# Kernel optimization log

Hardware: AMD Instinct MI355X
Metric: run time of the kernel (lower is better)

## Reference

```python
import jax, jax.numpy as jnp
import numpy as np

EMBED_DIM = 768
NUM_HEADS = 12
HEAD_DIM = EMBED_DIM // NUM_HEADS
B, T = 2, 2048


def setup_inputs() -> dict:
    key = jax.random.key(0)
    ks = jax.random.split(key, 11)
    s = 1.0 / np.sqrt(EMBED_DIM)
    return {
        "query": jax.random.normal(ks[0], (B, T, EMBED_DIM), jnp.float32),
        "key_in": jax.random.normal(ks[1], (B, T, EMBED_DIM), jnp.float32),
        "value": jax.random.normal(ks[2], (B, T, EMBED_DIM), jnp.float32),
        "Wq": jax.random.uniform(ks[3], (EMBED_DIM, EMBED_DIM), jnp.float32, -s, s),
        "bq": jnp.zeros((EMBED_DIM,), jnp.float32),
        "Wk": jax.random.uniform(ks[4], (EMBED_DIM, EMBED_DIM), jnp.float32, -s, s),
        "bk": jnp.zeros((EMBED_DIM,), jnp.float32),
        "Wv": jax.random.uniform(ks[5], (EMBED_DIM, EMBED_DIM), jnp.float32, -s, s),
        "bv": jnp.zeros((EMBED_DIM,), jnp.float32),
        "Wo": jax.random.uniform(ks[6], (EMBED_DIM, EMBED_DIM), jnp.float32, -s, s),
        "bo": jnp.zeros((EMBED_DIM,), jnp.float32),
    }


def reference(query, key_in, value, Wq, bq, Wk, bk, Wv, bv, Wo, bo):
    b, t, _ = query.shape

    def split_heads(x):  # [B,T,E] -> [B,H,T,Dh]
        return x.reshape(b, t, NUM_HEADS, HEAD_DIM).transpose(0, 2, 1, 3)

    Q = split_heads(query @ Wq + bq)
    K = split_heads(key_in @ Wk + bk)
    V = split_heads(value @ Wv + bv)

    scores = jnp.einsum("bhqd,bhkd->bhqk", Q, K) / np.sqrt(HEAD_DIM).astype(np.float32)
    attn = jax.nn.softmax(scores, axis=-1)
    out = jnp.einsum("bhqk,bhkd->bhqd", attn, V)  # [B,H,T,Dh]
    out = out.transpose(0, 2, 1, 3).reshape(b, t, EMBED_DIM)
    return out @ Wo + bo
```

## Files before the change

### kernel.cpp

```cpp
#include <hip/hip_runtime.h>
#include <math.h>

typedef __attribute__((ext_vector_type(4))) float  floatx4;
typedef __attribute__((ext_vector_type(16))) float f32x16;
typedef __attribute__((ext_vector_type(8))) short  short8;
typedef __attribute__((ext_vector_type(4))) short  short4v;
typedef __attribute__((ext_vector_type(8))) __bf16 bf16x8;
typedef __attribute__((ext_vector_type(4))) unsigned int uint4v;

#define E_DIM 768
#define T_DIM 2048
#define N_B   2
#define N_H   12
#define H_D   64
#define M_TOT 4096

#define Q_SCALE 0.1803368801111204f

#if __has_builtin(__builtin_amdgcn_exp2f)
#define EXP2F(x) __builtin_amdgcn_exp2f(x)
#else
#define EXP2F(x) exp2f(x)
#endif
#if __has_builtin(__builtin_amdgcn_rcpf)
#define RCPF(x) __builtin_amdgcn_rcpf(x)
#else
#define RCPF(x) (1.0f / (x))
#endif

__device__ __forceinline__ unsigned short f32_to_bf16(float f) {
  unsigned int u = __float_as_uint(f);
  u += 0x7fffu + ((u >> 16) & 1u);
  return (unsigned short)(u >> 16);
}

__device__ __forceinline__ void lds_barrier() {
  asm volatile("s_waitcnt lgkmcnt(0)\n\ts_barrier" ::: "memory");
}

__device__ __forceinline__ void gload_lds16(const unsigned short* g, unsigned short* l) {
  __builtin_amdgcn_global_load_lds(
      (const __attribute__((address_space(1))) unsigned int*)(const void*)g,
      (__attribute__((address_space(3))) unsigned int*)(void*)l, 16, 0, 0);
}

__device__ __forceinline__ unsigned int cvtpk_bf16(float lo, float hi) {
  unsigned int r;
  asm("v_cvt_pk_bf16_f32 %0, %1, %2" : "=v"(r) : "v"(lo), "v"(hi));
  return r;
}

__device__ __forceinline__ void perml32_swap(unsigned int& a, unsigned int& b) {
  asm volatile("v_permlane32_swap_b32 %0, %1" : "+v"(a), "+v"(b));
}

__global__ __launch_bounds__(256) void convert_x(const float* __restrict__ q,
                                                 const float* __restrict__ k,
                                                 const float* __restrict__ v,
                                                 unsigned short* __restrict__ Xb) {
  const int z = blockIdx.y;
  const float* src = (z == 0) ? q : (z == 1) ? k : v;
  size_t idx = ((size_t)blockIdx.x * 256 + threadIdx.x) * 4;
  float4 val = *reinterpret_cast<const float4*>(&src[idx]);
  short4v o;
  o[0] = (short)f32_to_bf16(val.x);
  o[1] = (short)f32_to_bf16(val.y);
  o[2] = (short)f32_to_bf16(val.z);
  o[3] = (short)f32_to_bf16(val.w);
  *reinterpret_cast<short4v*>(&Xb[(size_t)z * M_TOT * E_DIM + idx]) = o;
}

__global__ __launch_bounds__(256) void transpose_w4(const float* __restrict__ W0,
                                                    const float* __restrict__ W1,
                                                    const float* __restrict__ W2,
                                                    const float* __restrict__ W3,
                                                    unsigned short* __restrict__ Wt) {
  __shared__ float tile[32][33];
  const int z = blockIdx.z;
  const float* W = (z == 0) ? W0 : (z == 1) ? W1 : (z == 2) ? W2 : W3;
  unsigned short* dst = Wt + (size_t)z * E_DIM * E_DIM;
  int k0 = blockIdx.x * 32, n0 = blockIdx.y * 32;
  int tx = threadIdx.x & 31, ty = threadIdx.x >> 5;
  for (int i = 0; i < 4; i++)
    tile[ty + i * 8][tx] = W[(size_t)(k0 + ty + i * 8) * E_DIM + n0 + tx];
  __syncthreads();
  for (int i = 0; i < 4; i++)
    dst[(size_t)(n0 + ty + i * 8) * E_DIM + k0 + tx] = f32_to_bf16(tile[tx][ty + i * 8]);
}

__global__ __launch_bounds__(256) void gemm_qkv(const unsigned short* __restrict__ Xb,
                                                const unsigned short* __restrict__ WtAll,
                                                const float* __restrict__ bq,
                                                const float* __restrict__ bk,
                                                const float* __restrict__ bv,
                                                unsigned short* __restrict__ outQKV) {
  __shared__ unsigned short As[128 * 32];
  __shared__ unsigned short Bs[128 * 32];

  const int z = blockIdx.z;
  const unsigned short* A = Xb + (size_t)z * M_TOT * E_DIM;
  const float* bias = (z == 0) ? bq : (z == 1) ? bk : bv;
  const unsigned short* W = WtAll + (size_t)z * E_DIM * E_DIM;
  unsigned short* out = outQKV + (size_t)z * M_TOT * E_DIM;
  const float scale = (z == 0) ? Q_SCALE : 1.0f;

  const int tid = threadIdx.x;
  const int lane = tid & 63, wv = tid >> 6;
  const int m15 = lane & 15, quad = lane >> 4;
  const int wm = (wv & 1) * 64, wn = (wv >> 1) * 64;
  const int m0 = blockIdx.x * 128, n0 = blockIdx.y * 128;

  floatx4 acc[4][4] = {};
  const int srow = lane >> 2, scol = (lane & 3) * 8;

  for (int k0 = 0; k0 < E_DIM; k0 += 32) {
    for (int cc = 0; cc < 2; cc++) {
      int c = wv * 2 + cc;
      gload_lds16(&A[(size_t)(m0 + c * 16 + srow) * E_DIM + k0 + scol], &As[c * 512]);
      gload_lds16(&W[(size_t)(n0 + c * 16 + srow) * E_DIM + k0 + scol], &Bs[c * 512]);
    }
    __syncthreads();
    bf16x8 af[4], bfr[4];
    for (int i = 0; i < 4; i++)
      af[i] = *reinterpret_cast<const bf16x8*>(&As[(wm + i * 16 + m15) * 32 + quad * 8]);
    for (int j = 0; j < 4; j++)
      bfr[j] = *reinterpret_cast<const bf16x8*>(&Bs[(wn + j * 16 + m15) * 32 + quad * 8]);
    for (int i = 0; i < 4; i++)
      for (int j = 0; j < 4; j++)
        acc[i][j] = __builtin_amdgcn_mfma_f32_16x16x32_bf16(af[i], bfr[j], acc[i][j], 0, 0, 0);
    __syncthreads();
  }

  for (int i = 0; i < 4; i++)
    for (int j = 0; j < 4; j++) {
      int gn = n0 + wn + j * 16 + m15;
      int h = gn >> 6, d = gn & 63;
      float bso = bias[gn];
      for (int r = 0; r < 4; r++) {
        int gm = m0 + wm + i * 16 + quad * 4 + r;
        int bb = gm >> 11, tt = gm & 2047;
        float v = (acc[i][j][r] + bso) * scale;
        out[(((size_t)bb * N_H + h) * T_DIM + tt) * H_D + d] = f32_to_bf16(v);
      }
    }
}

__global__ __launch_bounds__(256) void transpose_v(const unsigned short* __restrict__ Vg_all,
                                                   unsigned short* __restrict__ VT) {
  __shared__ unsigned short tile[64 * 72];
  const int t0 = blockIdx.x * 64, h = blockIdx.y, bb = blockIdx.z;
  const unsigned short* Vg = Vg_all + (((size_t)bb * N_H + h) * T_DIM) * H_D;
  unsigned short* VTh = VT + (((size_t)bb * N_H + h) * H_D) * T_DIM;
  const int tid = threadIdx.x;
  const int tloc = tid & 63, d0 = (tid >> 6) * 16;

  short8 r0 = *reinterpret_cast<const short8*>(&Vg[(size_t)(t0 + tloc) * H_D + d0]);
  short8 r1 = *reinterpret_cast<const short8*>(&Vg[(size_t)(t0 + tloc) * H_D + d0 + 8]);
#pragma unroll
  for (int j = 0; j < 8; j++) {
    tile[(d0 + j) * 72 + tloc] = (unsigned short)r0[j];
    tile[(d0 + 8 + j) * 72 + tloc] = (unsigned short)r1[j];
  }
  __syncthreads();
  const int d = tid >> 2, ts = (tid & 3) * 16;
  short8 w0 = *reinterpret_cast<const short8*>(&tile[d * 72 + ts]);
  short8 w1 = *reinterpret_cast<const short8*>(&tile[d * 72 + ts + 8]);
  *reinterpret_cast<short8*>(&VTh[(size_t)d * T_DIM + t0 + ts]) = w0;
  *reinterpret_cast<short8*>(&VTh[(size_t)d * T_DIM + t0 + ts + 8]) = w1;
}

__global__ __launch_bounds__(64, 1) void attn(const unsigned short* __restrict__ QKV,
                                              const unsigned short* __restrict__ VT,
                                              unsigned short* __restrict__ ctx) {
  __shared__ unsigned short Ks[2][64 * 64];
  __shared__ unsigned short Vs[2][64 * 64];

  const int qt = blockIdx.x, h = blockIdx.y, bb = blockIdx.z;
  const size_t headoff = (((size_t)bb * N_H + h) * T_DIM) * H_D;
  const unsigned short* Qg = QKV + headoff;
  const unsigned short* Kg = QKV + (size_t)M_TOT * E_DIM + headoff;
  const unsigned short* VTg = VT + (((size_t)bb * N_H + h) * H_D) * T_DIM;

  const int lane = threadIdx.x;
  const int l31 = lane & 31, hi = lane >> 5, l7 = lane & 7;
  const int q0 = qt * 64;

  const int srow = lane >> 3;
  const int sslot = (lane & 7) ^ srow;
  const unsigned short* gK = Kg + (size_t)srow * H_D + sslot * 8;
  const unsigned short* gV = VTg + (size_t)srow * T_DIM + sslot * 8;

  bf16x8 aqA[4], aqB[4];
#pragma unroll
  for (int c = 0; c < 4; c++) {
    aqA[c] = *reinterpret_cast<const bf16x8*>(&Qg[(size_t)(q0 + l31) * H_D + c * 16 + hi * 8]);
    aqB[c] = *reinterpret_cast<const bf16x8*>(&Qg[(size_t)(q0 + 32 + l31) * H_D + c * 16 + hi * 8]);
  }

#pragma unroll
  for (int i = 0; i < 8; i++) {
    gload_lds16(gK + (size_t)(i * 8) * H_D, &Ks[0][i * 512]);
    gload_lds16(gV + (size_t)(i * 8) * T_DIM, &Vs[0][i * 512]);
  }
#pragma unroll
  for (int i = 0; i < 8; i++) {
    gload_lds16(gK + (size_t)(64 + i * 8) * H_D, &Ks[1][i * 512]);
    gload_lds16(gV + (size_t)(i * 8) * T_DIM + 64, &Vs[1][i * 512]);
  }
  asm volatile("s_waitcnt vmcnt(16)" ::: "memory");

  f32x16 oA0 = {}, oA1 = {}, oB0 = {}, oB1 = {};
  float laccA = 0.f, laccB = 0.f;
  bf16x8 paA0[2], paA1[2], paB0[2], paB1[2];

  auto QK = [&](const unsigned short* kb, f32x16& a0, f32x16& a1, f32x16& b0, f32x16& b1) {
#pragma unroll
    for (int c = 0; c < 4; c++) {
      const int slot = ((c << 1) | hi) ^ l7;
      bf16x8 k0 = *reinterpret_cast<const bf16x8*>(&kb[l31 * 64 + slot * 8]);
      bf16x8 k1 = *reinterpret_cast<const bf16x8*>(&kb[(32 + l31) * 64 + slot * 8]);
      a0 = __builtin_amdgcn_mfma_f32_32x32x16_bf16(k0, aqA[c], a0, 0, 0, 0);
      a1 = __builtin_amdgcn_mfma_f32_32x32x16_bf16(k1, aqA[c], a1, 0, 0, 0);
      b0 = __builtin_amdgcn_mfma_f32_32x32x16_bf16(k0, aqB[c], b0, 0, 0, 0);
      b1 = __builtin_amdgcn_mfma_f32_32x32x16_bf16(k1, aqB[c], b1, 0, 0, 0);
    }
  };
  auto PV = [&](const unsigned short* vb) {
#pragma unroll
    for (int cc = 0; cc < 2; cc++) {
      const int sl0 = ((cc << 1) | hi) ^ l7;
      const int sl1 = (4 + (cc << 1) + hi) ^ l7;
      bf16x8 v00 = *reinterpret_cast<const bf16x8*>(&vb[l31 * 64 + sl0 * 8]);
      bf16x8 v01 = *reinterpret_cast<const bf16x8*>(&vb[(32 + l31) * 64 + sl0 * 8]);
      bf16x8 v10 = *reinterpret_cast<const bf16x8*>(&vb[l31 * 64 + sl1 * 8]);
      bf16x8 v11 = *reinterpret_cast<const bf16x8*>(&vb[(32 + l31) * 64 + sl1 * 8]);
      oA0 = __builtin_amdgcn_mfma_f32_32x32x16_bf16(paA0[cc], v00, oA0, 0, 0, 0);
      oA1 = __builtin_amdgcn_mfma_f32_32x32x16_bf16(paA0[cc], v01, oA1, 0, 0, 0);
      oA0 = __builtin_amdgcn_mfma_f32_32x32x16_bf16(paA1[cc], v10, oA0, 0, 0, 0);
      oA1 = __builtin_amdgcn_mfma_f32_32x32x16_bf16(paA1[cc], v11, oA1, 0, 0, 0);
      oB0 = __builtin_amdgcn_mfma_f32_32x32x16_bf16(paB0[cc], v00, oB0, 0, 0, 0);
      oB1 = __builtin_amdgcn_mfma_f32_32x32x16_bf16(paB0[cc], v01, oB1, 0, 0, 0);
      oB0 = __builtin_amdgcn_mfma_f32_32x32x16_bf16(paB1[cc], v10, oB0, 0, 0, 0);
      oB1 = __builtin_amdgcn_mfma_f32_32x32x16_bf16(paB1[cc], v11, oB1, 0, 0, 0);
    }
  };
  auto PACK1 = [&](f32x16& s0, f32x16& s1, float& lacc, bf16x8* pl, bf16x8* ph) {
#pragma unroll
    for (int i = 0; i < 16; i++) { s0[i] = EXP2F(s0[i]); s1[i] = EXP2F(s1[i]); }
    float a0 = 0.f, a1 = 0.f, a2 = 0.f, a3 = 0.f;
#pragma unroll
    for (int i = 0; i < 16; i += 4) {
      a0 += s0[i]; a1 += s0[i + 1]; a2 += s0[i + 2]; a3 += s0[i + 3];
      a0 += s1[i]; a1 += s1[i + 1]; a2 += s1[i + 2]; a3 += s1[i + 3];
    }
    lacc += (a0 + a1) + (a2 + a3);
#pragma unroll
    for (int cc = 0; cc < 2; cc++) {
      {
        unsigned int x0 = cvtpk_bf16(s0[8 * cc + 0], s0[8 * cc + 1]);
        unsigned int x1 = cvtpk_bf16(s0[8 * cc + 2], s0[8 * cc + 3]);
        unsigned int y0 = cvtpk_bf16(s0[8 * cc + 4], s0[8 * cc + 5]);
        unsigned int y1 = cvtpk_bf16(s0[8 * cc + 6], s0[8 * cc + 7]);
        perml32_swap(x0, y0);
        perml32_swap(x1, y1);
        uint4v u; u[0] = x0; u[1] = x1; u[2] = y0; u[3] = y1;
        pl[cc] = __builtin_bit_cast(bf16x8, u);
      }
      {
        unsigned int x0 = cvtpk_bf16(s1[8 * cc + 0], s1[8 * cc + 1]);
        unsigned int x1 = cvtpk_bf16(s1[8 * cc + 2], s1[8 * cc + 3]);
        unsigned int y0 = cvtpk_bf16(s1[8 * cc + 4], s1[8 * cc + 5]);
        unsigned int y1 = cvtpk_bf16(s1[8 * cc + 6], s1[8 * cc + 7]);
        perml32_swap(x0, y0);
        perml32_swap(x1, y1);
        uint4v u; u[0] = x0; u[1] = x1; u[2] = y0; u[3] = y1;
        ph[cc] = __builtin_bit_cast(bf16x8, u);
      }
    }
  };

  {
    f32x16 sA0 = {}, sA1 = {}, sB0 = {}, sB1 = {};
    __builtin_amdgcn_s_setprio(1);
    QK(Ks[0], sA0, sA1, sB0, sB1);
    __builtin_amdgcn_s_setprio(0);
    asm volatile("s_waitcnt lgkmcnt(0)" ::: "memory");
#pragma unroll
    for (int i = 0; i < 8; i++)
      gload_lds16(gK + (size_t)(128 + i * 8) * H_D, &Ks[0][i * 512]);
    PACK1(sA0, sA1, laccA, paA0, paA1);
    PACK1(sB0, sB1, laccB, paB0, paB1);
    asm volatile("s_waitcnt vmcnt(8)" ::: "memory");
  }

  for (int kt = 1; kt <= 30; ++kt) {
    f32x16 sA0 = {}, sA1 = {}, sB0 = {}, sB1 = {};
    __builtin_amdgcn_s_setprio(1);
    QK(Ks[kt & 1], sA0, sA1, sB0, sB1);
    PV(Vs[(kt - 1) & 1]);
    __builtin_amdgcn_s_setprio(0);
    asm volatile("s_waitcnt lgkmcnt(0)" ::: "memory");
    if (kt < 30) {
      const int nk = kt + 2;
#pragma unroll
      for (int i = 0; i < 8; i++)
        gload_lds16(gK + (size_t)(nk * 64 + i * 8) * H_D, &Ks[kt & 1][i * 512]);
    }
    {
      const int nv = kt + 1;
#pragma unroll
      for (int i = 0; i < 8; i++)
        gload_lds16(gV + (size_t)(i * 8) * T_DIM + nv * 64, &Vs[nv & 1][i * 512]);
    }
    PACK1(sA0, sA1, laccA, paA0, paA1);
    PACK1(sB0, sB1, laccB, paB0, paB1);
    if (kt < 30) asm volatile("s_waitcnt vmcnt(16)" ::: "memory");
    else         asm volatile("s_waitcnt vmcnt(8)" ::: "memory");
  }

  {
    f32x16 sA0 = {}, sA1 = {}, sB0 = {}, sB1 = {};
    __builtin_amdgcn_s_setprio(1);
    QK(Ks[1], sA0, sA1, sB0, sB1);
    PV(Vs[0]);
    __builtin_amdgcn_s_setprio(0);
    PACK1(sA0, sA1, laccA, paA0, paA1);
    PACK1(sB0, sB1, laccB, paB0, paB1);
    asm volatile("s_waitcnt vmcnt(0)" ::: "memory");
    __builtin_amdgcn_s_setprio(1);
    PV(Vs[1]);
    __builtin_amdgcn_s_setprio(0);
  }

  float ltA = laccA + __shfl_xor(laccA, 32, 64);
  float rlA = RCPF(ltA);
  float ltB = laccB + __shfl_xor(laccB, 32, 64);
  float rlB = RCPF(ltB);
  const size_t obase = ((size_t)bb * T_DIM + q0) * E_DIM + (size_t)h * H_D;
#pragma unroll
  for (int r = 0; r < 16; r++) {
    const int qr = (r & 3) + 8 * (r >> 2) + 4 * hi;
    float ra = __shfl(rlA, qr, 64);
    ctx[obase + (size_t)qr * E_DIM + l31]      = f32_to_bf16(oA0[r] * ra);
    ctx[obase + (size_t)qr * E_DIM + 32 + l31] = f32_to_bf16(oA1[r] * ra);
    float rb = __shfl(rlB, qr, 64);
    ctx[obase + (size_t)(32 + qr) * E_DIM + l31]      = f32_to_bf16(oB0[r] * rb);
    ctx[obase + (size_t)(32 + qr) * E_DIM + 32 + l31] = f32_to_bf16(oB1[r] * rb);
  }
}

__global__ __launch_bounds__(256) void gemm_out(const unsigned short* __restrict__ Actx,
                                                const unsigned short* __restrict__ Wt,
                                                const float* __restrict__ bias,
                                                float* __restrict__ out) {
  __shared__ unsigned short As[64 * 32];
  __shared__ unsigned short Bs[128 * 32];

  const int tid = threadIdx.x;
  const int lane = tid & 63, wv = tid >> 6;
  const int m15 = lane & 15, quad = lane >> 4;
  const int wm = (wv & 1) * 32, wn = (wv >> 1) * 64;
  const int m0 = blockIdx.x * 64, n0 = blockIdx.y * 128;

  floatx4 acc[2][4] = {};
  const int srow = lane >> 2, scol = (lane & 3) * 8;

  for (int k0 = 0; k0 < E_DIM; k0 += 32) {
    gload_lds16(&Actx[(size_t)(m0 + wv * 16 + srow) * E_DIM + k0 + scol], &As[wv * 512]);
    for (int cc = 0; cc < 2; cc++) {
      int c = wv * 2 + cc;
      gload_lds16(&Wt[(size_t)(n0 + c * 16 + srow) * E_DIM + k0 + scol], &Bs[c * 512]);
    }
    __syncthreads();
    bf16x8 af[2], bfr[4];
    for (int i = 0; i < 2; i++)
      af[i] = *reinterpret_cast<const bf16x8*>(&As[(wm + i * 16 + m15) * 32 + quad * 8]);
    for (int j = 0; j < 4; j++)
      bfr[j] = *reinterpret_cast<const bf16x8*>(&Bs[(wn + j * 16 + m15) * 32 + quad * 8]);
    for (int i = 0; i < 2; i++)
      for (int j = 0; j < 4; j++)
        acc[i][j] = __builtin_amdgcn_mfma_f32_16x16x32_bf16(af[i], bfr[j], acc[i][j], 0, 0, 0);
    __syncthreads();
  }

  for (int i = 0; i < 2; i++)
    for (int j = 0; j < 4; j++) {
      int gn = n0 + wn + j * 16 + m15;
      float bso = bias[gn];
      for (int r = 0; r < 4; r++) {
        int gm = m0 + wm + i * 16 + quad * 4 + r;
        out[(size_t)gm * E_DIM + gn] = acc[i][j][r] + bso;
      }
    }
}

extern "C" void kernel_launch(void* const* d_in, const int* in_sizes, int n_in,
                              void* d_out, int out_size, void* d_ws, size_t ws_size,
                              hipStream_t stream) {
  const float* query  = (const float*)d_in[0];
  const float* key_in = (const float*)d_in[1];
  const float* value  = (const float*)d_in[2];
  const float* Wq = (const float*)d_in[3];
  const float* bq = (const float*)d_in[4];
  const float* Wk = (const float*)d_in[5];
  const float* bk = (const float*)d_in[6];
  const float* Wv = (const float*)d_in[7];
  const float* bv = (const float*)d_in[8];
  const float* Wo = (const float*)d_in[9];
  const float* bo = (const float*)d_in[10];
  float* out = (float*)d_out;

  unsigned short* ws  = (unsigned short*)d_ws;
  unsigned short* Wt  = ws;
  unsigned short* Xb  = Wt + (size_t)4 * E_DIM * E_DIM;
  unsigned short* QKV = Xb + (size_t)3 * M_TOT * E_DIM;
  unsigned short* VT  = QKV + (size_t)3 * M_TOT * E_DIM;
  unsigned short* ctx = VT + (size_t)N_B * N_H * H_D * T_DIM;

  dim3 tb(256);
  convert_x<<<dim3(M_TOT * E_DIM / 1024, 3), tb, 0, stream>>>(query, key_in, value, Xb);
  transpose_w4<<<dim3(24, 24, 4), tb, 0, stream>>>(Wq, Wk, Wv, Wo, Wt);

  gemm_qkv<<<dim3(32, 6, 3), tb, 0, stream>>>(Xb, Wt, bq, bk, bv, QKV);
  transpose_v<<<dim3(32, 12, 2), tb, 0, stream>>>(QKV + (size_t)2 * M_TOT * E_DIM, VT);
  attn<<<dim3(32, 12, 2), dim3(64), 0, stream>>>(QKV, VT, ctx);
  gemm_out<<<dim3(64, 6), tb, 0, stream>>>(ctx, Wt + (size_t)3 * E_DIM * E_DIM, bo, out);
  (void)in_sizes; (void)n_in; (void)out_size; (void)ws_size;
}
```

Measured before the change: 198.1 us.

## Split attention KV range across two blocks with atomic accumulation and combine kernel

Each attention block now covers only half of the key/value tiles, so twice as many single-wave blocks are launched to fill more of the GPU. Partial unnormalized outputs and row sums are accumulated into fp32 buffers with atomicAdd. A new combine kernel then normalizes the result and converts it to bf16 for the output GEMM. The fp32 buffer is zeroed inside the V-transpose kernel and reuses the Xb workspace. The cost is extra atomic traffic, a zeroing pass and one more kernel launch. The approach relies on the softmax not using a per-block running max, so the two halves add linearly.

```diff
diff --git a/kernel.cpp b/kernel.cpp
--- a/kernel.cpp
+++ b/kernel.cpp
@@ -14,6 +14,8 @@
 #define N_H   12
 #define H_D   64
 #define M_TOT 4096
+
+#define KV_TILES_PER_BLOCK 16
 
 #define Q_SCALE 0.1803368801111204f
 
@@ -32,10 +34,6 @@
   unsigned int u = __float_as_uint(f);
   u += 0x7fffu + ((u >> 16) & 1u);
   return (unsigned short)(u >> 16);
-}
-
-__device__ __forceinline__ void lds_barrier() {
-  asm volatile("s_waitcnt lgkmcnt(0)\n\ts_barrier" ::: "memory");
 }
 
 __device__ __forceinline__ void gload_lds16(const unsigned short* g, unsigned short* l) {
@@ -146,7 +144,8 @@
 }
 
 __global__ __launch_bounds__(256) void transpose_v(const unsigned short* __restrict__ Vg_all,
-                                                   unsigned short* __restrict__ VT) {
+                                                   unsigned short* __restrict__ VT,
+                                                   float* __restrict__ Oz) {
   __shared__ unsigned short tile[64 * 72];
   const int t0 = blockIdx.x * 64, h = blockIdx.y, bb = blockIdx.z;
   const unsigned short* Vg = Vg_all + (((size_t)bb * N_H + h) * T_DIM) * H_D;
@@ -154,6 +153,14 @@
   const int tid = threadIdx.x;
   const int tloc = tid & 63, d0 = (tid >> 6) * 16;
 
+  {
+    const unsigned int gid = ((blockIdx.z * (unsigned)N_H + blockIdx.y) * 32 + blockIdx.x) * 256 + tid;
+    float4* Z = reinterpret_cast<float4*>(Oz);
+    const float4 z4 = {0.f, 0.f, 0.f, 0.f};
+    for (size_t i = gid; i < (size_t)((M_TOT * E_DIM + M_TOT * N_H) / 4); i += 196608)
+      Z[i] = z4;
+  }
+
   short8 r0 = *reinterpret_cast<const short8*>(&Vg[(size_t)(t0 + tloc) * H_D + d0]);
   short8 r1 = *reinterpret_cast<const short8*>(&Vg[(size_t)(t0 + tloc) * H_D + d0 + 8]);
 #pragma unroll
@@ -171,11 +178,14 @@
 
 __global__ __launch_bounds__(64, 1) void attn(const unsigned short* __restrict__ QKV,
                                               const unsigned short* __restrict__ VT,
-                                              unsigned short* __restrict__ ctx) {
+                                              float* __restrict__ O,
+                                              float* __restrict__ L) {
   __shared__ unsigned short Ks[2][64 * 64];
   __shared__ unsigned short Vs[2][64 * 64];
 
-  const int qt = blockIdx.x, h = blockIdx.y, bb = blockIdx.z;
+  const int qt = blockIdx.x, h = blockIdx.y;
+  const int bb = blockIdx.z >> 1, half = blockIdx.z & 1;
+  const int tb = half * KV_TILES_PER_BLOCK;
   const size_t headoff = (((size_t)bb * N_H + h) * T_DIM) * H_D;
   const unsigned short* Qg = QKV + headoff;
   const unsigned short* Kg = QKV + (size_t)M_TOT * E_DIM + headoff;
@@ -199,13 +209,13 @@
 
 #pragma unroll
   for (int i = 0; i < 8; i++) {
-    gload_lds16(gK + (size_t)(i * 8) * H_D, &Ks[0][i * 512]);
-    gload_lds16(gV + (size_t)(i * 8) * T_DIM, &Vs[0][i * 512]);
+    gload_lds16(gK + (size_t)((tb + 0) * 64 + i * 8) * H_D, &Ks[0][i * 512]);
+    gload_lds16(gV + (size_t)(i * 8) * T_DIM + (tb + 0) * 64, &Vs[0][i * 512]);
   }
 #pragma unroll
   for (int i = 0; i < 8; i++) {
-    gload_lds16(gK + (size_t)(64 + i * 8) * H_D, &Ks[1][i * 512]);
-    gload_lds16(gV + (size_t)(i * 8) * T_DIM + 64, &Vs[1][i * 512]);
+    gload_lds16(gK + (size_t)((tb + 1) * 64 + i * 8) * H_D, &Ks[1][i * 512]);
+    gload_lds16(gV + (size_t)(i * 8) * T_DIM + (tb + 1) * 64, &Vs[1][i * 512]);
   }
   asm volatile("s_waitcnt vmcnt(16)" ::: "memory");
 
@@ -287,66 +297,84 @@
     asm volatile("s_waitcnt lgkmcnt(0)" ::: "memory");
 #pragma unroll
     for (int i = 0; i < 8; i++)
-      gload_lds16(gK + (size_t)(128 + i * 8) * H_D, &Ks[0][i * 512]);
+      gload_lds16(gK + (size_t)((tb + 2) * 64 + i * 8) * H_D, &Ks[0][i * 512]);
     PACK1(sA0, sA1, laccA, paA0, paA1);
     PACK1(sB0, sB1, laccB, paB0, paB1);
     asm volatile("s_waitcnt vmcnt(8)" ::: "memory");
   }
 
-  for (int kt = 1; kt <= 30; ++kt) {
+  for (int kt = 1; kt <= KV_TILES_PER_BLOCK - 2; ++kt) {
     f32x16 sA0 = {}, sA1 = {}, sB0 = {}, sB1 = {};
     __builtin_amdgcn_s_setprio(1);
     QK(Ks[kt & 1], sA0, sA1, sB0, sB1);
     PV(Vs[(kt - 1) & 1]);
     __builtin_amdgcn_s_setprio(0);
     asm volatile("s_waitcnt lgkmcnt(0)" ::: "memory");
-    if (kt < 30) {
+    if (kt < KV_TILES_PER_BLOCK - 2) {
       const int nk = kt + 2;
 #pragma unroll
       for (int i = 0; i < 8; i++)
-        gload_lds16(gK + (size_t)(nk * 64 + i * 8) * H_D, &Ks[kt & 1][i * 512]);
+        gload_lds16(gK + (size_t)((tb + nk) * 64 + i * 8) * H_D, &Ks[kt & 1][i * 512]);
     }
     {
       const int nv = kt + 1;
 #pragma unroll
       for (int i = 0; i < 8; i++)
-        gload_lds16(gV + (size_t)(i * 8) * T_DIM + nv * 64, &Vs[nv & 1][i * 512]);
+        gload_lds16(gV + (size_t)(i * 8) * T_DIM + (tb + nv) * 64, &Vs[nv & 1][i * 512]);
     }
     PACK1(sA0, sA1, laccA, paA0, paA1);
     PACK1(sB0, sB1, laccB, paB0, paB1);
-    if (kt < 30) asm volatile("s_waitcnt vmcnt(16)" ::: "memory");
-    else         asm volatile("s_waitcnt vmcnt(8)" ::: "memory");
+    if (kt < KV_TILES_PER_BLOCK - 2)
+      asm volatile("s_waitcnt vmcnt(16)" ::: "memory");
+    else
+      asm volatile("s_waitcnt vmcnt(8)" ::: "memory");
   }
 
   {
     f32x16 sA0 = {}, sA1 = {}, sB0 = {}, sB1 = {};
     __builtin_amdgcn_s_setprio(1);
-    QK(Ks[1], sA0, sA1, sB0, sB1);
-    PV(Vs[0]);
+    QK(Ks[(KV_TILES_PER_BLOCK - 1) & 1], sA0, sA1, sB0, sB1);
+    PV(Vs[(KV_TILES_PER_BLOCK - 2) & 1]);
     __builtin_amdgcn_s_setprio(0);
     PACK1(sA0, sA1, laccA, paA0, paA1);
     PACK1(sB0, sB1, laccB, paB0, paB1);
     asm volatile("s_waitcnt vmcnt(0)" ::: "memory");
     __builtin_amdgcn_s_setprio(1);
-    PV(Vs[1]);
+    PV(Vs[(KV_TILES_PER_BLOCK - 1) & 1]);
     __builtin_amdgcn_s_setprio(0);
   }
 
   float ltA = laccA + __shfl_xor(laccA, 32, 64);
-  float rlA = RCPF(ltA);
   float ltB = laccB + __shfl_xor(laccB, 32, 64);
-  float rlB = RCPF(ltB);
   const size_t obase = ((size_t)bb * T_DIM + q0) * E_DIM + (size_t)h * H_D;
 #pragma unroll
   for (int r = 0; r < 16; r++) {
     const int qr = (r & 3) + 8 * (r >> 2) + 4 * hi;
-    float ra = __shfl(rlA, qr, 64);
-    ctx[obase + (size_t)qr * E_DIM + l31]      = f32_to_bf16(oA0[r] * ra);
-    ctx[obase + (size_t)qr * E_DIM + 32 + l31] = f32_to_bf16(oA1[r] * ra);
-    float rb = __shfl(rlB, qr, 64);
-    ctx[obase + (size_t)(32 + qr) * E_DIM + l31]      = f32_to_bf16(oB0[r] * rb);
-    ctx[obase + (size_t)(32 + qr) * E_DIM + 32 + l31] = f32_to_bf16(oB1[r] * rb);
-  }
+    atomicAdd(&O[obase + (size_t)qr * E_DIM + l31], oA0[r]);
+    atomicAdd(&O[obase + (size_t)qr * E_DIM + 32 + l31], oA1[r]);
+    atomicAdd(&O[obase + (size_t)(32 + qr) * E_DIM + l31], oB0[r]);
+    atomicAdd(&O[obase + (size_t)(32 + qr) * E_DIM + 32 + l31], oB1[r]);
+  }
+  if (hi == 0) {
+    atomicAdd(&L[((size_t)bb * T_DIM + q0 + l31) * N_H + h], ltA);
+    atomicAdd(&L[((size_t)bb * T_DIM + q0 + 32 + l31) * N_H + h], ltB);
+  }
+}
+
+__global__ __launch_bounds__(256) void combine(const float* __restrict__ O,
+                                               const float* __restrict__ L,
+                                               unsigned short* __restrict__ ctx) {
+  const size_t idx = (size_t)blockIdx.x * 256 + threadIdx.x;
+  const size_t m = idx / (E_DIM / 4);
+  const int e0 = (int)(idx % (E_DIM / 4)) * 4;
+  const float rl = RCPF(L[m * N_H + (e0 >> 6)]);
+  float4 o = *reinterpret_cast<const float4*>(&O[m * E_DIM + e0]);
+  short4v c;
+  c[0] = (short)f32_to_bf16(o.x * rl);
+  c[1] = (short)f32_to_bf16(o.y * rl);
+  c[2] = (short)f32_to_bf16(o.z * rl);
+  c[3] = (short)f32_to_bf16(o.w * rl);
+  *reinterpret_cast<short4v*>(&ctx[m * E_DIM + e0]) = c;
 }
 
 __global__ __launch_bounds__(256) void gemm_out(const unsigned short* __restrict__ Actx,
@@ -416,14 +444,17 @@
   unsigned short* QKV = Xb + (size_t)3 * M_TOT * E_DIM;
   unsigned short* VT  = QKV + (size_t)3 * M_TOT * E_DIM;
   unsigned short* ctx = VT + (size_t)N_B * N_H * H_D * T_DIM;
+  float* Obuf = (float*)Xb;
+  float* Lbuf = Obuf + (size_t)M_TOT * E_DIM;
 
   dim3 tb(256);
   convert_x<<<dim3(M_TOT * E_DIM / 1024, 3), tb, 0, stream>>>(query, key_in, value, Xb);
   transpose_w4<<<dim3(24, 24, 4), tb, 0, stream>>>(Wq, Wk, Wv, Wo, Wt);
 
   gemm_qkv<<<dim3(32, 6, 3), tb, 0, stream>>>(Xb, Wt, bq, bk, bv, QKV);
-  transpose_v<<<dim3(32, 12, 2), tb, 0, stream>>>(QKV + (size_t)2 * M_TOT * E_DIM, VT);
-  attn<<<dim3(32, 12, 2), dim3(64), 0, stream>>>(QKV, VT, ctx);
+  transpose_v<<<dim3(32, 12, 2), tb, 0, stream>>>(QKV + (size_t)2 * M_TOT * E_DIM, VT, Obuf);
+  attn<<<dim3(32, 12, 4), dim3(64), 0, stream>>>(QKV, VT, Obuf, Lbuf);
+  combine<<<dim3(M_TOT * E_DIM / 1024), tb, 0, stream>>>(Obuf, Lbuf, ctx);
   gemm_out<<<dim3(64, 6), tb, 0, stream>>>(ctx, Wt + (size_t)3 * E_DIM * E_DIM, bo, out);
   (void)in_sizes; (void)n_in; (void)out_size; (void)ws_size;
 }
```

Result: slower. 221.4 us (+11.8%).

## Merge prep kernels and widen QKV GEMM K-tile with swizzled LDS layout

Applied to the files above, without the earlier changes.

Folds the input conversion and weight transpose into one prep launch, which drops a kernel launch. In the QKV GEMM, the K step grows from 32 to 64, halving the number of barrier pairs per tile, and the LDS layout gets an XOR swizzle to avoid bank conflicts on fragment reads. Blocks are also remapped with a swizzled order across M and N tiles for better L2 locality. The cost is double the LDS per block, which may reduce occupancy.

```diff
diff --git a/kernel.cpp b/kernel.cpp
--- a/kernel.cpp
+++ b/kernel.cpp
@@ -34,10 +34,6 @@
   return (unsigned short)(u >> 16);
 }
 
-__device__ __forceinline__ void lds_barrier() {
-  asm volatile("s_waitcnt lgkmcnt(0)\n\ts_barrier" ::: "memory");
-}
-
 __device__ __forceinline__ void gload_lds16(const unsigned short* g, unsigned short* l) {
   __builtin_amdgcn_global_load_lds(
       (const __attribute__((address_space(1))) unsigned int*)(const void*)g,
@@ -54,38 +50,41 @@
   asm volatile("v_permlane32_swap_b32 %0, %1" : "+v"(a), "+v"(b));
 }
 
-__global__ __launch_bounds__(256) void convert_x(const float* __restrict__ q,
-                                                 const float* __restrict__ k,
-                                                 const float* __restrict__ v,
-                                                 unsigned short* __restrict__ Xb) {
-  const int z = blockIdx.y;
-  const float* src = (z == 0) ? q : (z == 1) ? k : v;
-  size_t idx = ((size_t)blockIdx.x * 256 + threadIdx.x) * 4;
-  float4 val = *reinterpret_cast<const float4*>(&src[idx]);
-  short4v o;
-  o[0] = (short)f32_to_bf16(val.x);
-  o[1] = (short)f32_to_bf16(val.y);
-  o[2] = (short)f32_to_bf16(val.z);
-  o[3] = (short)f32_to_bf16(val.w);
-  *reinterpret_cast<short4v*>(&Xb[(size_t)z * M_TOT * E_DIM + idx]) = o;
-}
-
-__global__ __launch_bounds__(256) void transpose_w4(const float* __restrict__ W0,
-                                                    const float* __restrict__ W1,
-                                                    const float* __restrict__ W2,
-                                                    const float* __restrict__ W3,
-                                                    unsigned short* __restrict__ Wt) {
+__global__ __launch_bounds__(256) void prep(const float* __restrict__ q,
+                                            const float* __restrict__ k,
+                                            const float* __restrict__ v,
+                                            const float* __restrict__ W0,
+                                            const float* __restrict__ W1,
+                                            const float* __restrict__ W2,
+                                            const float* __restrict__ W3,
+                                            unsigned short* __restrict__ Xb,
+                                            unsigned short* __restrict__ Wt) {
   __shared__ float tile[32][33];
-  const int z = blockIdx.z;
-  const float* W = (z == 0) ? W0 : (z == 1) ? W1 : (z == 2) ? W2 : W3;
-  unsigned short* dst = Wt + (size_t)z * E_DIM * E_DIM;
-  int k0 = blockIdx.x * 32, n0 = blockIdx.y * 32;
-  int tx = threadIdx.x & 31, ty = threadIdx.x >> 5;
-  for (int i = 0; i < 4; i++)
-    tile[ty + i * 8][tx] = W[(size_t)(k0 + ty + i * 8) * E_DIM + n0 + tx];
-  __syncthreads();
-  for (int i = 0; i < 4; i++)
-    dst[(size_t)(n0 + ty + i * 8) * E_DIM + k0 + tx] = f32_to_bf16(tile[tx][ty + i * 8]);
+  const int b = blockIdx.x, tid = threadIdx.x;
+  if (b < 9216) {
+    const int z = b / 3072, bx = b - z * 3072;
+    const float* src = (z == 0) ? q : (z == 1) ? k : v;
+    size_t idx = ((size_t)bx * 256 + tid) * 4;
+    float4 val = *reinterpret_cast<const float4*>(&src[idx]);
+    short4v o;
+    o[0] = (short)f32_to_bf16(val.x);
+    o[1] = (short)f32_to_bf16(val.y);
+    o[2] = (short)f32_to_bf16(val.z);
+    o[3] = (short)f32_to_bf16(val.w);
+    *reinterpret_cast<short4v*>(&Xb[(size_t)z * M_TOT * E_DIM + idx]) = o;
+  } else {
+    const int t = b - 9216;
+    const int z = t / 576, rem = t - z * 576;
+    const int k0 = (rem / 24) * 32, n0 = (rem % 24) * 32;
+    const float* W = (z == 0) ? W0 : (z == 1) ? W1 : (z == 2) ? W2 : W3;
+    unsigned short* dst = Wt + (size_t)z * E_DIM * E_DIM;
+    const int tx = tid & 31, ty = tid >> 5;
+    for (int i = 0; i < 4; i++)
+      tile[ty + i * 8][tx] = W[(size_t)(k0 + ty + i * 8) * E_DIM + n0 + tx];
+    __syncthreads();
+    for (int i = 0; i < 4; i++)
+      dst[(size_t)(n0 + ty + i * 8) * E_DIM + k0 + tx] = f32_to_bf16(tile[tx][ty + i * 8]);
+  }
 }
 
 __global__ __launch_bounds__(256) void gemm_qkv(const unsigned short* __restrict__ Xb,
@@ -94,8 +93,8 @@
                                                 const float* __restrict__ bk,
                                                 const float* __restrict__ bv,
                                                 unsigned short* __restrict__ outQKV) {
-  __shared__ unsigned short As[128 * 32];
-  __shared__ unsigned short Bs[128 * 32];
+  __shared__ unsigned short As[128 * 64];
+  __shared__ unsigned short Bs[128 * 64];
 
   const int z = blockIdx.z;
   const unsigned short* A = Xb + (size_t)z * M_TOT * E_DIM;
@@ -104,30 +103,46 @@
   unsigned short* out = outQKV + (size_t)z * M_TOT * E_DIM;
   const float scale = (z == 0) ? Q_SCALE : 1.0f;
 
+  const int f = blockIdx.x;
+  const int swz = (f & 7) * 24 + (f >> 3);
+  const int m0 = (swz % 32) * 128, n0 = (swz / 32) * 128;
+
   const int tid = threadIdx.x;
   const int lane = tid & 63, wv = tid >> 6;
   const int m15 = lane & 15, quad = lane >> 4;
   const int wm = (wv & 1) * 64, wn = (wv >> 1) * 64;
-  const int m0 = blockIdx.x * 128, n0 = blockIdx.y * 128;
+
+  const int srow = lane >> 3, sslot = (lane & 7) ^ srow;
 
   floatx4 acc[4][4] = {};
-  const int srow = lane >> 2, scol = (lane & 3) * 8;
-
-  for (int k0 = 0; k0 < E_DIM; k0 += 32) {
-    for (int cc = 0; cc < 2; cc++) {
-      int c = wv * 2 + cc;
-      gload_lds16(&A[(size_t)(m0 + c * 16 + srow) * E_DIM + k0 + scol], &As[c * 512]);
-      gload_lds16(&W[(size_t)(n0 + c * 16 + srow) * E_DIM + k0 + scol], &Bs[c * 512]);
+
+  for (int k0 = 0; k0 < E_DIM; k0 += 64) {
+#pragma unroll
+    for (int i = 0; i < 4; i++) {
+      const int rb = wv * 32 + i * 8;
+      gload_lds16(&A[(size_t)(m0 + rb + srow) * E_DIM + k0 + sslot * 8], &As[rb * 64]);
+      gload_lds16(&W[(size_t)(n0 + rb + srow) * E_DIM + k0 + sslot * 8], &Bs[rb * 64]);
     }
     __syncthreads();
-    bf16x8 af[4], bfr[4];
-    for (int i = 0; i < 4; i++)
-      af[i] = *reinterpret_cast<const bf16x8*>(&As[(wm + i * 16 + m15) * 32 + quad * 8]);
-    for (int j = 0; j < 4; j++)
-      bfr[j] = *reinterpret_cast<const bf16x8*>(&Bs[(wn + j * 16 + m15) * 32 + quad * 8]);
-    for (int i = 0; i < 4; i++)
-      for (int j = 0; j < 4; j++)
-        acc[i][j] = __builtin_amdgcn_mfma_f32_16x16x32_bf16(af[i], bfr[j], acc[i][j], 0, 0, 0);
+#pragma unroll
+    for (int kk = 0; kk < 2; kk++) {
+      bf16x8 af[4], bfr[4];
+#pragma unroll
+      for (int i = 0; i < 4; i++) {
+        const int r = wm + i * 16 + m15;
+        af[i] = *reinterpret_cast<const bf16x8*>(&As[r * 64 + (((kk << 2) | quad) ^ (r & 7)) * 8]);
+      }
+#pragma unroll
+      for (int j = 0; j < 4; j++) {
+        const int r = wn + j * 16 + m15;
+        bfr[j] = *reinterpret_cast<const bf16x8*>(&Bs[r * 64 + (((kk << 2) | quad) ^ (r & 7)) * 8]);
+      }
+#pragma unroll
+      for (int i = 0; i < 4; i++)
+#pragma unroll
+        for (int j = 0; j < 4; j++)
+          acc[i][j] = __builtin_amdgcn_mfma_f32_16x16x32_bf16(af[i], bfr[j], acc[i][j], 0, 0, 0);
+    }
     __syncthreads();
   }
 
@@ -418,10 +433,8 @@
   unsigned short* ctx = VT + (size_t)N_B * N_H * H_D * T_DIM;
 
   dim3 tb(256);
-  convert_x<<<dim3(M_TOT * E_DIM / 1024, 3), tb, 0, stream>>>(query, key_in, value, Xb);
-  transpose_w4<<<dim3(24, 24, 4), tb, 0, stream>>>(Wq, Wk, Wv, Wo, Wt);
-
-  gemm_qkv<<<dim3(32, 6, 3), tb, 0, stream>>>(Xb, Wt, bq, bk, bv, QKV);
+  prep<<<dim3(11520), tb, 0, stream>>>(query, key_in, value, Wq, Wk, Wv, Wo, Xb, Wt);
+  gemm_qkv<<<dim3(192, 1, 3), tb, 0, stream>>>(Xb, Wt, bq, bk, bv, QKV);
   transpose_v<<<dim3(32, 12, 2), tb, 0, stream>>>(QKV + (size_t)2 * M_TOT * E_DIM, VT);
   attn<<<dim3(32, 12, 2), dim3(64), 0, stream>>>(QKV, VT, ctx);
   gemm_out<<<dim3(64, 6), tb, 0, stream>>>(ctx, Wt + (size_t)3 * E_DIM * E_DIM, bo, out);
```

Result: slower. 206.9 us (+4.4%).
